# Kernel optimization log

Measured on AMD Instinct MI355X. Metric: run time of the kernel, lower is better.

Reference implementation:

```python
import jax, jax.numpy as jnp
import numpy as np
from functools import partial

V, E, H, HD, OUT = 50000, 256, 512, 256, 2
B, T = 64, 512

def setup_inputs() -> dict:
    key = jax.random.key(0)
    ks = jax.random.split(key, 32)
    def lin(kw, kb, out_d, in_d):
        s = 1.0 / np.sqrt(in_d)
        return (jax.random.uniform(kw, (out_d, in_d), jnp.float32, -s, s),
                jax.random.uniform(kb, (out_d,), jnp.float32, -s, s))
    Wir, bir = lin(ks[0], ks[1], H, E)
    Whr, bhr = lin(ks[2], ks[3], H, H)
    Wif, bif = lin(ks[4], ks[5], H, E)
    Whf, bhf = lin(ks[6], ks[7], H, H)
    Wig, big = lin(ks[8], ks[9], H, E)
    Whg, bhg = lin(ks[10], ks[11], H, H)
    Wio, bio = lin(ks[12], ks[13], H, E)
    Who, bho = lin(ks[14], ks[15], H, H)
    W_ol, b_ol = lin(ks[16], ks[17], HD, H)          # fc_out_lstm
    W_fc, b_fc = lin(ks[18], ks[19], OUT, H + HD)    # fc_out_attent
    emb = jax.random.normal(ks[20], (V, E), jnp.float32)
    W_att = jax.random.normal(ks[21], (HD, H), jnp.float32) * 0.02  # torch init is zeros; use small random so attention is non-trivial
    b_att = jnp.zeros((H,), jnp.float32)
    input_words = jax.random.randint(ks[22], (B, T), 0, V, dtype=jnp.int64)
    return dict(input_words=input_words, emb=emb,
                Wir=Wir, bir=bir, Whr=Whr, bhr=bhr,
                Wif=Wif, bif=bif, Whf=Whf, bhf=bhf,
                Wig=Wig, big=big, Whg=Whg, bhg=bhg,
                Wio=Wio, bio=bio, Who=Who, bho=bho,
                W_att=W_att, b_att=b_att, W_ol=W_ol, b_ol=b_ol,
                W_fc=W_fc, b_fc=b_fc)

def reference(input_words, emb, Wir, bir, Whr, bhr, Wif, bif, Whf, bhf,
              Wig, big, Whg, bhg, Wio, bio, Who, bho,
              W_att, b_att, W_ol, b_ol, W_fc, b_fc):
    b, t = input_words.shape
    h0 = jnp.zeros((b, Whr.shape[0]), emb.dtype)
    c0 = jnp.zeros_like(h0)
    x = emb[input_words].transpose(1, 0, 2)  # [T,B,E]
    # Precompute all input projections as big GEMMs (same math, fused over time)
    pr = jnp.einsum('tbe,he->tbh', x, Wir) + bir
    pf = jnp.einsum('tbe,he->tbh', x, Wif) + bif
    pg = jnp.einsum('tbe,he->tbh', x, Wig) + big
    po = jnp.einsum('tbe,he->tbh', x, Wio) + bio
    def step(carry, pres):
        h, c = carry
        xr, xf, xg, xo = pres
        rt = jax.nn.sigmoid(xr + h @ Whr.T + bhr)
        ft = jax.nn.sigmoid(xf + h @ Whf.T + bhf)
        gt = jnp.tanh(xg + h @ Whg.T + bhg)
        ot = jax.nn.sigmoid(xo + h @ Who.T + bho)
        c = ft * c + rt * gt
        h = ot * jnp.tanh(c)
        return (h, c), h
    (h_last, _), hs = jax.lax.scan(step, (h0, c0), (pr, pf, pg, po))
    final_hidden = h_last @ W_ol.T + b_ol                 # [B,HD]
    outputs = hs.transpose(1, 2, 0)                       # [B,H,T]
    score = final_hidden @ W_att + b_att                  # [B,H]
    att_score = jnp.einsum('bh,bht->bt', score, outputs)  # [B,T]
    dist = jax.nn.softmax(att_score, axis=-1)
    att_out = jnp.einsum('bht,bt->bh', outputs, dist)     # [B,H]
    out = jnp.concatenate([final_hidden, att_out], axis=1) @ W_fc.T + b_fc
    return jax.nn.sigmoid(out), h_last
```

## Files before the change

kernel.cpp:

```cpp
#include <hip/hip_runtime.h>
#include <cstdint>
#include <cstddef>

typedef unsigned short u16;
typedef unsigned int u32;
typedef unsigned long long u64;
typedef __attribute__((ext_vector_type(8))) short bfrag8;
typedef __attribute__((ext_vector_type(4))) float f32x4;

#define NB 64
#define NT 512
#define NE 256
#define NH 512
#define NWGW 128
#define NBLK 256
#define WSTR 408

__device__ __forceinline__ float bf2f(u16 b) { return __uint_as_float(((unsigned)b) << 16); }
__device__ __forceinline__ u16 f2bf(float f) {
  unsigned u = __float_as_uint(f);
  u += 0x7fffu + ((u >> 16) & 1u);
  return (u16)(u >> 16);
}
__device__ __forceinline__ float fsigm(float x) { return 1.0f / (1.0f + __expf(-x)); }
__device__ __forceinline__ float ftanh(float x) { return 2.0f / (1.0f + __expf(-2.0f * x)) - 1.0f; }

__device__ __forceinline__ void split1(float v, u16& h, u16& l) {
  h = f2bf(v);
  float r = v - bf2f(h);
  l = f2bf(r);
}
__device__ __forceinline__ void split8(const float* p, bfrag8& hi, bfrag8& lo) {
#pragma unroll
  for (int i = 0; i < 8; ++i) {
    u16 h, l; split1(p[i], h, l);
    hi[i] = (short)h; lo[i] = (short)l;
  }
}

__device__ __forceinline__ void unpack8(uint4 q, float* o) {
  o[0] = __uint_as_float(q.x << 16); o[1] = __uint_as_float(q.x & 0xffff0000u);
  o[2] = __uint_as_float(q.y << 16); o[3] = __uint_as_float(q.y & 0xffff0000u);
  o[4] = __uint_as_float(q.z << 16); o[5] = __uint_as_float(q.z & 0xffff0000u);
  o[6] = __uint_as_float(q.w << 16); o[7] = __uint_as_float(q.w & 0xffff0000u);
}

__global__ __launch_bounds__(64) void stage_weights(
    const float* __restrict__ Whr, const float* __restrict__ Whf,
    const float* __restrict__ Whg, const float* __restrict__ Who,
    const float* __restrict__ Wir, const float* __restrict__ Wif,
    const float* __restrict__ Wig, const float* __restrict__ Wio,
    const float* __restrict__ bhr, const float* __restrict__ bhf,
    const float* __restrict__ bhg, const float* __restrict__ bho,
    const float* __restrict__ bir, const float* __restrict__ bif,
    const float* __restrict__ big_, const float* __restrict__ bio,
    u16* __restrict__ wbuf, float* __restrict__ bias_s)
{
  const int wg = blockIdx.x;
  const int lane = threadIdx.x;
  const int colq = lane & 15;
  const int koff = (lane >> 4) * 8;
  const int gate = colq >> 2;
  const int gu = wg * 4 + (colq & 3);
  const float* wh = (gate == 0) ? Whr : (gate == 1) ? Whf : (gate == 2) ? Whg : Who;
  const float* wi = (gate == 0) ? Wir : (gate == 1) ? Wif : (gate == 2) ? Wig : Wio;
  u16* wb = wbuf + (size_t)(wg * 64 + lane) * 48 * 8;
  const float* whp = wh + (size_t)gu * NH + koff;
  const float* wip = wi + (size_t)gu * NE + koff;
#pragma unroll
  for (int kt = 0; kt < 16; ++kt) {
    bfrag8 hi, lo; split8(whp + kt * 32, hi, lo);
    *(bfrag8*)(wb + kt * 8) = hi;
    *(bfrag8*)(wb + (16 + kt) * 8) = lo;
  }
#pragma unroll
  for (int kt = 0; kt < 8; ++kt) {
    bfrag8 hi, lo; split8(wip + kt * 32, hi, lo);
    *(bfrag8*)(wb + (32 + kt) * 8) = hi;
    *(bfrag8*)(wb + (40 + kt) * 8) = lo;
  }
  if (lane < 16) {
    int g2 = lane >> 2, u2 = lane & 3, gu2 = wg * 4 + u2;
    const float* bh = (g2 == 0) ? bhr : (g2 == 1) ? bhf : (g2 == 2) ? bhg : bho;
    const float* bi = (g2 == 0) ? bir : (g2 == 1) ? bif : (g2 == 2) ? big_ : bio;
    bias_s[wg * 16 + lane] = bh[gu2] + bi[gu2];
  }
}

__global__ __launch_bounds__(256, 1) void lstm_persist(
    const int* __restrict__ words,
    const float* __restrict__ emb,
    const u16* __restrict__ wbuf,
    const float* __restrict__ bias_s,
    u64* __restrict__ hbuf,
    u16* __restrict__ hs_all,
    float* __restrict__ hlast,
    u32* __restrict__ slots)
{
  const int G    = blockIdx.x >> 6;
  const int ib   = blockIdx.x & 63;
  const int tid  = threadIdx.x;
  const int lane = tid & 63;
  const int wave = tid >> 6;
  const int colq = lane & 15;
  const int koff = (lane >> 4) * 8;
  const int arow = 16 * G + colq;

  __shared__ u16 wlds[2 * 64 * WSTR];
  __shared__ float pl[4 * 16 * 34];
  __shared__ float biasLds[32];

  if (wave < 2) {
    const u16* src = wbuf + (size_t)((ib * 2 + wave) * 64 + lane) * 384;
    u16* dst = wlds + (size_t)(wave * 64 + lane) * WSTR;
#pragma unroll
    for (int i = 0; i < 48; ++i)
      *(bfrag8*)(dst + i * 8) = *(const bfrag8*)(src + i * 8);
  }
  if (tid < 32) biasLds[tid] = bias_s[ib * 32 + tid];
  __syncthreads();

  const bool is64 = ((words[1] | words[3] | words[5] | words[7]) == 0);
  const int r_loc = tid >> 3;
  const int uo    = tid & 7;
  float creg = 0.0f;

  f32x4 xa[2], xb[2];
  {
    int widx = arow * NT + 0;
    int wd = is64 ? words[2 * widx] : words[widx];
    const float* xs = emb + (size_t)wd * NE + wave * 64 + koff;
    xa[0] = *(const f32x4*)(xs);      xb[0] = *(const f32x4*)(xs + 4);
    xa[1] = *(const f32x4*)(xs + 32); xb[1] = *(const f32x4*)(xs + 36);
  }

  const u16* wl0 = wlds + (size_t)lane * WSTR;
  const u16* wl1 = wlds + (size_t)(64 + lane) * WSTR;
  const size_t pstore = (size_t)G * 4096 + (size_t)(ib >> 4) * 1024
                      + (size_t)((ib >> 2) & 3) * 256 + (size_t)(uo >> 1) * 64
                      + (size_t)((ib & 3) * 16 + r_loc);
  u32* postp = slots + (G * 64 + ib) * 16;
  const u32* pollp = slots + (G * 64 + 16 * wave + colq) * 16;

  for (int t = 1; t <= NT; ++t) {
    bfrag8 xh[2], xl[2];
#pragma unroll
    for (int xt = 0; xt < 2; ++xt)
#pragma unroll
      for (int i = 0; i < 4; ++i) {
        u16 h, l;
        split1(xa[xt][i], h, l); xh[xt][i] = (short)h;     xl[xt][i] = (short)l;
        split1(xb[xt][i], h, l); xh[xt][4 + i] = (short)h; xl[xt][4 + i] = (short)l;
      }

    if (t < NT) {
      int widx = arow * NT + t;
      int wd = is64 ? words[2 * widx] : words[widx];
      const float* xs = emb + (size_t)wd * NE + wave * 64 + koff;
      xa[0] = *(const f32x4*)(xs);      xb[0] = *(const f32x4*)(xs + 4);
      xa[1] = *(const f32x4*)(xs + 32); xb[1] = *(const f32x4*)(xs + 36);
    }

    f32x4 acc0 = {0.f, 0.f, 0.f, 0.f};
    f32x4 acc1 = {0.f, 0.f, 0.f, 0.f};

#pragma unroll
    for (int xt = 0; xt < 2; ++xt) {
      int f = 2 * wave + xt;
      bfrag8 wih = *(const bfrag8*)(wl0 + (32 + f) * 8);
      bfrag8 wil = *(const bfrag8*)(wl0 + (40 + f) * 8);
      acc0 = __builtin_amdgcn_mfma_f32_16x16x32_bf16(xh[xt], wih, acc0, 0, 0, 0);
      acc0 = __builtin_amdgcn_mfma_f32_16x16x32_bf16(xl[xt], wih, acc0, 0, 0, 0);
      acc0 = __builtin_amdgcn_mfma_f32_16x16x32_bf16(xh[xt], wil, acc0, 0, 0, 0);
    }
#pragma unroll
    for (int xt = 0; xt < 2; ++xt) {
      int f = 2 * wave + xt;
      bfrag8 wih = *(const bfrag8*)(wl1 + (32 + f) * 8);
      bfrag8 wil = *(const bfrag8*)(wl1 + (40 + f) * 8);
      acc1 = __builtin_amdgcn_mfma_f32_16x16x32_bf16(xh[xt], wih, acc1, 0, 0, 0);
      acc1 = __builtin_amdgcn_mfma_f32_16x16x32_bf16(xl[xt], wih, acc1, 0, 0, 0);
      acc1 = __builtin_amdgcn_mfma_f32_16x16x32_bf16(xh[xt], wil, acc1, 0, 0, 0);
    }

    if (t > 1) {
      const u32 need = (u32)(t - 1);
      u32 v;
      do {
        v = __hip_atomic_load(pollp, __ATOMIC_RELAXED, __HIP_MEMORY_SCOPE_AGENT);
      } while (!__all((int)(v >= need)));
      asm volatile("" ::: "memory");

      const u64* hb = hbuf + ((size_t)(((t - 1) & 1) * 16 + G * 4 + wave)) * 1024 + lane;
      u64 q[16];
#pragma unroll
      for (int i = 0; i < 16; ++i)
        q[i] = __hip_atomic_load(hb + (size_t)i * 64, __ATOMIC_RELAXED, __HIP_MEMORY_SCOPE_AGENT);

#pragma unroll
      for (int ktl = 0; ktl < 4; ++ktl) {
        bfrag8 ah, al;
#pragma unroll
        for (int p = 0; p < 4; ++p) {
          u64 vq = q[ktl * 4 + p];
          u32 w0 = (u32)vq, w1 = (u32)(vq >> 32);
          ah[2 * p]     = (short)(w0 >> 16); al[2 * p]     = (short)(w0 & 0xffffu);
          ah[2 * p + 1] = (short)(w1 >> 16); al[2 * p + 1] = (short)(w1 & 0xffffu);
        }
        int f = 4 * wave + ktl;
        bfrag8 whh0 = *(const bfrag8*)(wl0 + f * 8);
        bfrag8 whl0 = *(const bfrag8*)(wl0 + (16 + f) * 8);
        bfrag8 whh1 = *(const bfrag8*)(wl1 + f * 8);
        bfrag8 whl1 = *(const bfrag8*)(wl1 + (16 + f) * 8);
        acc0 = __builtin_amdgcn_mfma_f32_16x16x32_bf16(ah, whh0, acc0, 0, 0, 0);
        acc1 = __builtin_amdgcn_mfma_f32_16x16x32_bf16(ah, whh1, acc1, 0, 0, 0);
        acc0 = __builtin_amdgcn_mfma_f32_16x16x32_bf16(al, whh0, acc0, 0, 0, 0);
        acc1 = __builtin_amdgcn_mfma_f32_16x16x32_bf16(al, whh1, acc1, 0, 0, 0);
        acc0 = __builtin_amdgcn_mfma_f32_16x16x32_bf16(ah, whl0, acc0, 0, 0, 0);
        acc1 = __builtin_amdgcn_mfma_f32_16x16x32_bf16(ah, whl1, acc1, 0, 0, 0);
      }
    }

    {
      int rb = (lane >> 4) << 2;
#pragma unroll
      for (int r = 0; r < 4; ++r) {
        pl[(wave * 16 + rb + r) * 34 + colq] = acc0[r];
        pl[(wave * 16 + rb + r) * 34 + 16 + colq] = acc1[r];
      }
    }
    __syncthreads();

    if (tid < 128) {
      int clb = ((uo >> 2) << 4) + (uo & 3);
      const float* pr = pl + r_loc * 34;
      float xr = biasLds[clb], xf = biasLds[clb + 4];
      float xg = biasLds[clb + 8], xo = biasLds[clb + 12];
#pragma unroll
      for (int w = 0; w < 4; ++w) {
        const float* pw = pr + w * 16 * 34;
        xr += pw[clb]; xf += pw[clb + 4]; xg += pw[clb + 8]; xo += pw[clb + 12];
      }
      float rg = fsigm(xr), fg = fsigm(xf), gg = ftanh(xg), og = fsigm(xo);
      creg = fg * creg + rg * gg;
      float hv = og * ftanh(creg);
      u16 hhi, hlo; split1(hv, hhi, hlo);
      u32 hval = ((u32)hhi << 16) | (u32)hlo;
      u32 pv = (u32)__shfl_xor((int)hval, 1);
      int grow = 16 * G + r_loc;
      int gcol = 8 * ib + uo;
      if ((uo & 1) == 0) {
        u64 e = (u64)hval | ((u64)pv << 32);
        __hip_atomic_store(hbuf + (size_t)(t & 1) * 16384 + pstore, e,
                           __ATOMIC_RELAXED, __HIP_MEMORY_SCOPE_AGENT);
        u32 hspack = (u32)hhi | (pv & 0xffff0000u);
        *(u32*)&hs_all[(size_t)(t - 1) * (NB * NH) + (size_t)grow * NH + gcol] = hspack;
      }
      if (t == NT) hlast[grow * NH + gcol] = hv;
    }

    __syncthreads();
    if (tid == 0)
      __hip_atomic_store(postp, (u32)t, __ATOMIC_RELAXED, __HIP_MEMORY_SCOPE_AGENT);
  }
}

__global__ __launch_bounds__(256) void post_kernel(
    const float* __restrict__ hlast,
    const u16* __restrict__ hs,
    const float* __restrict__ W_ol, const float* __restrict__ b_ol,
    const float* __restrict__ W_att, const float* __restrict__ b_att,
    const float* __restrict__ W_fc, const float* __restrict__ b_fc,
    float* __restrict__ out)
{
  int b = blockIdx.x, tid = threadIdx.x;
  __shared__ float hl[NH], fh[256], sc[NH], att[NT], ao[NH], red[256];

  for (int i = tid; i < NH; i += 256) {
    float hv = hlast[b * NH + i];
    hl[i] = hv;
    out[128 + b * NH + i] = hv;
  }
  __syncthreads();

  {
    float s = b_ol[tid];
    const float* w = W_ol + (size_t)tid * NH;
    for (int k = 0; k < NH; k += 4) {
      f32x4 q = *(const f32x4*)(w + k);
      s += q[0] * hl[k] + q[1] * hl[k + 1] + q[2] * hl[k + 2] + q[3] * hl[k + 3];
    }
    fh[tid] = s;
  }
  __syncthreads();

  for (int h = tid; h < NH; h += 256) {
    float s = b_att[h];
    for (int j = 0; j < 256; ++j) s += fh[j] * W_att[(size_t)j * NH + h];
    sc[h] = s;
  }
  __syncthreads();

  for (int t = tid; t < NT; t += 256) {
    const u16* row = hs + ((size_t)t * NB + b) * NH;
    float s = 0.f;
    for (int k = 0; k < NH; k += 8) {
      uint4 q = *(const uint4*)(row + k);
      float tmp[8]; unpack8(q, tmp);
#pragma unroll
      for (int j = 0; j < 8; ++j) s += tmp[j] * sc[k + j];
    }
    att[t] = s;
  }
  __syncthreads();

  float l0 = att[tid], l1 = att[tid + 256];
  red[tid] = fmaxf(l0, l1);
  __syncthreads();
  for (int s = 128; s > 0; s >>= 1) { if (tid < s) red[tid] = fmaxf(red[tid], red[tid + s]); __syncthreads(); }
  float mx = red[0];
  __syncthreads();
  float e0 = __expf(l0 - mx), e1 = __expf(l1 - mx);
  red[tid] = e0 + e1;
  __syncthreads();
  for (int s = 128; s > 0; s >>= 1) { if (tid < s) red[tid] += red[tid + s]; __syncthreads(); }
  float inv = 1.0f / red[0];
  __syncthreads();
  att[tid] = e0 * inv;
  att[tid + 256] = e1 * inv;
  __syncthreads();

  {
    float a0 = 0.f, a1 = 0.f;
    for (int t = 0; t < NT; ++t) {
      float d = att[t];
      const u16* row = hs + ((size_t)t * NB + b) * NH;
      a0 += d * bf2f(row[tid]);
      a1 += d * bf2f(row[tid + 256]);
    }
    ao[tid] = a0;
    ao[tid + 256] = a1;
  }
  __syncthreads();

#pragma unroll
  for (int o = 0; o < 2; ++o) {
    float part = 0.f;
    for (int i = tid; i < 768; i += 256) {
      float v = (i < 256) ? fh[i] : ao[i - 256];
      part += v * W_fc[o * 768 + i];
    }
    red[tid] = part;
    __syncthreads();
    for (int s = 128; s > 0; s >>= 1) { if (tid < s) red[tid] += red[tid + s]; __syncthreads(); }
    if (tid == 0) out[b * 2 + o] = fsigm(red[0] + b_fc[o]);
    __syncthreads();
  }
}

extern "C" void kernel_launch(void* const* d_in, const int* in_sizes, int n_in,
                              void* d_out, int out_size, void* d_ws, size_t ws_size,
                              hipStream_t stream) {
  const int* words  = (const int*)d_in[0];
  const float* emb  = (const float*)d_in[1];
  const float* Wir  = (const float*)d_in[2];  const float* bir = (const float*)d_in[3];
  const float* Whr  = (const float*)d_in[4];  const float* bhr = (const float*)d_in[5];
  const float* Wif  = (const float*)d_in[6];  const float* bif = (const float*)d_in[7];
  const float* Whf  = (const float*)d_in[8];  const float* bhf = (const float*)d_in[9];
  const float* Wig  = (const float*)d_in[10]; const float* big_ = (const float*)d_in[11];
  const float* Whg  = (const float*)d_in[12]; const float* bhg = (const float*)d_in[13];
  const float* Wio  = (const float*)d_in[14]; const float* bio = (const float*)d_in[15];
  const float* Who  = (const float*)d_in[16]; const float* bho = (const float*)d_in[17];
  const float* W_att = (const float*)d_in[18]; const float* b_att = (const float*)d_in[19];
  const float* W_ol  = (const float*)d_in[20]; const float* b_ol  = (const float*)d_in[21];
  const float* W_fc  = (const float*)d_in[22]; const float* b_fc  = (const float*)d_in[23];

  uint8_t* ws = (uint8_t*)d_ws;
  u16* hs       = (u16*)ws;
  size_t off    = (size_t)33554432;
  u16* wbuf     = (u16*)(ws + off);   off += 6291456;
  float* bias_s = (float*)(ws + off); off += 8192;
  u64* hbuf     = (u64*)(ws + off);   off += 262144;
  float* hlast  = (float*)(ws + off); off += 131072;
  u32* slots    = (u32*)(ws + off);

  hipMemsetAsync(slots, 0, 16384, stream);

  stage_weights<<<dim3(NWGW), dim3(64), 0, stream>>>(
      Whr, Whf, Whg, Who, Wir, Wif, Wig, Wio,
      bhr, bhf, bhg, bho, bir, bif, big_, bio, wbuf, bias_s);

  lstm_persist<<<dim3(NBLK), dim3(256), 0, stream>>>(
      words, emb, wbuf, bias_s, hbuf, hs, hlast, slots);

  post_kernel<<<dim3(NB), dim3(256), 0, stream>>>(hlast, hs, W_ol, b_ol, W_att, b_att,
                                                  W_fc, b_fc, (float*)d_out);
}
```

Before: 1.632 ms.

## Issue early poll load, defer embedding prefetch, restructure attention score reads

```diff
diff --git a/kernel.cpp b/kernel.cpp
--- a/kernel.cpp
+++ b/kernel.cpp
@@ -143,6 +143,12 @@
   const u32* pollp = slots + (G * 64 + 16 * wave + colq) * 16;
 
   for (int t = 1; t <= NT; ++t) {
+    const u32 need = (u32)(t - 1);
+
+    u32 pv0 = 0;
+    if (t > 1)
+      pv0 = __hip_atomic_load(pollp, __ATOMIC_RELAXED, __HIP_MEMORY_SCOPE_AGENT);
+
     bfrag8 xh[2], xl[2];
 #pragma unroll
     for (int xt = 0; xt < 2; ++xt)
@@ -152,14 +158,6 @@
         split1(xa[xt][i], h, l); xh[xt][i] = (short)h;     xl[xt][i] = (short)l;
         split1(xb[xt][i], h, l); xh[xt][4 + i] = (short)h; xl[xt][4 + i] = (short)l;
       }
-
-    if (t < NT) {
-      int widx = arow * NT + t;
-      int wd = is64 ? words[2 * widx] : words[widx];
-      const float* xs = emb + (size_t)wd * NE + wave * 64 + koff;
-      xa[0] = *(const f32x4*)(xs);      xb[0] = *(const f32x4*)(xs + 4);
-      xa[1] = *(const f32x4*)(xs + 32); xb[1] = *(const f32x4*)(xs + 36);
-    }
 
     f32x4 acc0 = {0.f, 0.f, 0.f, 0.f};
     f32x4 acc1 = {0.f, 0.f, 0.f, 0.f};
@@ -183,20 +181,31 @@
       acc1 = __builtin_amdgcn_mfma_f32_16x16x32_bf16(xh[xt], wil, acc1, 0, 0, 0);
     }
 
+    u64 q[16];
     if (t > 1) {
-      const u32 need = (u32)(t - 1);
-      u32 v;
-      do {
-        v = __hip_atomic_load(pollp, __ATOMIC_RELAXED, __HIP_MEMORY_SCOPE_AGENT);
-      } while (!__all((int)(v >= need)));
+      u32 a = pv0;
+      u32 bfl = __hip_atomic_load(pollp, __ATOMIC_RELAXED, __HIP_MEMORY_SCOPE_AGENT);
+      while (!__all((int)(a >= need))) {
+        a = bfl;
+        bfl = __hip_atomic_load(pollp, __ATOMIC_RELAXED, __HIP_MEMORY_SCOPE_AGENT);
+      }
       asm volatile("" ::: "memory");
 
       const u64* hb = hbuf + ((size_t)(((t - 1) & 1) * 16 + G * 4 + wave)) * 1024 + lane;
-      u64 q[16];
 #pragma unroll
       for (int i = 0; i < 16; ++i)
         q[i] = __hip_atomic_load(hb + (size_t)i * 64, __ATOMIC_RELAXED, __HIP_MEMORY_SCOPE_AGENT);
-
+    }
+
+    if (t < NT) {
+      int widx = arow * NT + t;
+      int wd = is64 ? words[2 * widx] : words[widx];
+      const float* xs = emb + (size_t)wd * NE + wave * 64 + koff;
+      xa[0] = *(const f32x4*)(xs);      xb[0] = *(const f32x4*)(xs + 4);
+      xa[1] = *(const f32x4*)(xs + 32); xb[1] = *(const f32x4*)(xs + 36);
+    }
+
+    if (t > 1) {
 #pragma unroll
       for (int ktl = 0; ktl < 4; ++ktl) {
         bfrag8 ah, al;
@@ -275,6 +284,7 @@
 {
   int b = blockIdx.x, tid = threadIdx.x;
   __shared__ float hl[NH], fh[256], sc[NH], att[NT], ao[NH], red[256];
+  __shared__ u16 rowbuf[16 * 520];
 
   for (int i = tid; i < NH; i += 256) {
     float hv = hlast[b * NH + i];
@@ -301,18 +311,33 @@
   }
   __syncthreads();
 
-  for (int t = tid; t < NT; t += 256) {
-    const u16* row = hs + ((size_t)t * NB + b) * NH;
-    float s = 0.f;
-    for (int k = 0; k < NH; k += 8) {
-      uint4 q = *(const uint4*)(row + k);
-      float tmp[8]; unpack8(q, tmp);
-#pragma unroll
-      for (int j = 0; j < 8; ++j) s += tmp[j] * sc[k + j];
-    }
-    att[t] = s;
-  }
-  __syncthreads();
+  {
+    int r = tid >> 4, p = tid & 15;
+    for (int t0 = 0; t0 < NT; t0 += 16) {
+      const u16* src = hs + ((size_t)(t0 + r) * NB + b) * NH + p * 32;
+      uint4 v0 = *(const uint4*)(src);
+      uint4 v1 = *(const uint4*)(src + 8);
+      uint4 v2 = *(const uint4*)(src + 16);
+      uint4 v3 = *(const uint4*)(src + 24);
+      u16* dst = rowbuf + r * 520 + p * 32;
+      *(uint4*)(dst) = v0; *(uint4*)(dst + 8) = v1;
+      *(uint4*)(dst + 16) = v2; *(uint4*)(dst + 24) = v3;
+      __syncthreads();
+      const u16* row = rowbuf + r * 520 + p * 32;
+      float s = 0.f;
+      for (int k = 0; k < 32; k += 8) {
+        uint4 qv = *(const uint4*)(row + k);
+        float tmp[8]; unpack8(qv, tmp);
+        const float* scv = &sc[p * 32 + k];
+#pragma unroll
+        for (int j = 0; j < 8; ++j) s += tmp[j] * scv[j];
+      }
+      s += __shfl_xor(s, 1); s += __shfl_xor(s, 2);
+      s += __shfl_xor(s, 4); s += __shfl_xor(s, 8);
+      if (p == 0) att[t0 + r] = s;
+      __syncthreads();
+    }
+  }
 
   float l0 = att[tid], l1 = att[tid + 256];
   red[tid] = fmaxf(l0, l1);
```

Result: slower. 1.871 ms (+14.6%).
